# Kernel tuning notes

Measured on AMD Instinct MI355X. Metric: run time of the kernel, lower is better.

## Reference

```python
import jax, jax.numpy as jnp
import numpy as np

N_NODES = 10000
N_EDGES = 640000
D = 128
N_LAYERS = 4


def setup_inputs() -> dict:
    key = jax.random.key(0)
    k1, k2, k3, k4, k5 = jax.random.split(key, 5)
    node_feats = jax.random.normal(k1, (N_NODES, D), dtype=jnp.float32)
    src = jax.random.randint(k2, (N_EDGES,), 0, N_NODES, dtype=jnp.int32)
    dst = jax.random.randint(k3, (N_EDGES,), 0, N_NODES, dtype=jnp.int32)
    # stacked per-layer Linear params (all layers are 128 -> 128)
    Ws = jax.random.normal(k4, (N_LAYERS, D, D), dtype=jnp.float32) / np.sqrt(D).astype(np.float32)
    bs = jax.random.normal(k5, (N_LAYERS, D), dtype=jnp.float32) * 0.01
    return {"node_feats": node_feats, "src": src, "dst": dst, "Ws": Ws, "bs": bs}


def reference(node_feats, src, dst, Ws, bs):
    # Each GCN_layer: h = Linear(x); h = sum_{u in N(v)} h_u  (copy_u/sum)
    # dgl.add_self_loop => aggregate includes the node's own h, i.e. + h.
    # activation = relu; dropout is identity in eval; no batchnorm / residual.
    def step(h, params):
        W, b = params
        hl = h @ W + b                                   # [N, D] dense GEMM
        msgs = hl[src]                                   # [E, D] gather
        agg = jax.ops.segment_sum(msgs, dst, num_segments=N_NODES) + hl  # scatter-sum + self-loop
        return jax.nn.relu(agg), None

    h, _ = jax.lax.scan(step, node_feats, (Ws, bs))
    return h
```

## Files before the change

### kernel.cpp

```cpp
#include <hip/hip_runtime.h>
#include <hip/hip_bf16.h>

#define N_NODES 10000
#define N_EDGES 640000
#define D 128
#define N_LAYERS 4

#define NBINS 79
#define BIN_CAP 10240
#define POISON 0xAAAAAAAAu
#define A_LD 136

typedef unsigned uv4 __attribute__((ext_vector_type(4)));
typedef short bf16x8 __attribute__((ext_vector_type(8)));
typedef float f32x4 __attribute__((ext_vector_type(4)));
typedef float f32x2 __attribute__((ext_vector_type(2)));


__global__ __launch_bounds__(256) void binA_wt_kernel(const int* __restrict__ src,
                                                      const int* __restrict__ dst,
                                                      unsigned* __restrict__ binCursor,
                                                      unsigned* __restrict__ binbuf,
                                                      const float* __restrict__ W,
                                                      unsigned short* __restrict__ Wt) {
    __shared__ int cnt[NBINS];
    __shared__ int gbase[NBINS];
    const int t = threadIdx.x;
    const int b = blockIdx.x;

    if (b >= 250) {
        const int g = (b - 250) * 256 + t;
        const int e0 = g * 8;
        const int l = e0 >> 14;
        const int r = e0 & 16383;
        const int n = r >> 7;
        const int k0 = r & 127;
        union { bf16x8 v; __hip_bfloat16 h[8]; } pk;
#pragma unroll
        for (int j = 0; j < 8; ++j)
            pk.h[j] = __float2bfloat16(W[l * 16384 + (k0 + j) * 128 + n]);
        *(bf16x8*)(Wt + e0) = pk.v;
        return;
    }

    if (t < NBINS) cnt[t] = 0;
    __syncthreads();

    const int e0 = b * 2560;
    unsigned key[10];
    int bin[10], pos[10];
#pragma unroll
    for (int j = 0; j < 10; ++j) {
        int e = e0 + j * 256 + t;
        int d = dst[e];
        int s = src[e];
        key[j] = ((unsigned)d << 14) | (unsigned)s;
        bin[j] = d >> 7;
        pos[j] = atomicAdd(&cnt[bin[j]], 1);
    }
    __syncthreads();
    if (t < NBINS) {
        unsigned old = atomicAdd(&binCursor[t], (unsigned)cnt[t]);
        gbase[t] = (int)(old - POISON);
    }
    __syncthreads();
#pragma unroll
    for (int j = 0; j < 10; ++j) {
        int p = gbase[bin[j]] + pos[j];
        if (p >= 0 && p < BIN_CAP) binbuf[bin[j] * BIN_CAP + p] = key[j];
    }
}


__global__ __launch_bounds__(256) void binB_gemm0_kernel(
        const unsigned* __restrict__ binbuf, const unsigned* __restrict__ binCursor,
        int* __restrict__ begs, int* __restrict__ degs,
        unsigned short* __restrict__ csr16,
        const float* __restrict__ hf, const unsigned short* __restrict__ WtL,
        const float* __restrict__ bias, unsigned short* __restrict__ hl) {
    __shared__ unsigned buf[BIN_CAP];
    __shared__ int deg[128], base[128], cur[128];
    const int b = blockIdx.x;
    const int t = threadIdx.x;

    if (b >= NBINS) {
        const int wave = t >> 6;
        const int lane = t & 63;
        const int ln = lane & 15;
        const int q = lane >> 4;
        const int row0 = (b - NBINS) * 64 + wave * 16;

        int m = row0 + ln;
        if (m > N_NODES - 1) m = N_NODES - 1;

        f32x4 acc[8];
#pragma unroll
        for (int n0 = 0; n0 < 8; ++n0) acc[n0] = (f32x4){0.f, 0.f, 0.f, 0.f};

#pragma unroll
        for (int k0 = 0; k0 < 128; k0 += 32) {
            float4 f0 = *(const float4*)(hf + (size_t)m * D + k0 + q * 8);
            float4 f1 = *(const float4*)(hf + (size_t)m * D + k0 + q * 8 + 4);
            union { bf16x8 v; __hip_bfloat16 b8[8]; } pk;
            pk.b8[0] = __float2bfloat16(f0.x); pk.b8[1] = __float2bfloat16(f0.y);
            pk.b8[2] = __float2bfloat16(f0.z); pk.b8[3] = __float2bfloat16(f0.w);
            pk.b8[4] = __float2bfloat16(f1.x); pk.b8[5] = __float2bfloat16(f1.y);
            pk.b8[6] = __float2bfloat16(f1.z); pk.b8[7] = __float2bfloat16(f1.w);
            bf16x8 a = pk.v;
#pragma unroll
            for (int n0 = 0; n0 < 8; ++n0) {
                bf16x8 bb = *(const bf16x8*)(WtL + (size_t)(n0 * 16 + ln) * D + k0 + q * 8);
                acc[n0] = __builtin_amdgcn_mfma_f32_16x16x32_bf16(a, bb, acc[n0], 0, 0, 0);
            }
        }

#pragma unroll
        for (int n0 = 0; n0 < 8; ++n0) {
            float bv = bias[n0 * 16 + ln];
#pragma unroll
            for (int r = 0; r < 4; ++r) {
                int row = row0 + q * 4 + r;
                if (row < N_NODES) {
                    __hip_bfloat16 o = __float2bfloat16(acc[n0][r] + bv);
                    hl[(size_t)row * D + n0 * 16 + ln] = *(unsigned short*)&o;
                }
            }
        }
        return;
    }

    int m = (int)(binCursor[b] - POISON);
    if (m > BIN_CAP) m = BIN_CAP;
    if (m < 0) m = 0;

    if (t < 128) deg[t] = 0;
    __syncthreads();

    for (int i = t; i < m; i += 256) {
        unsigned k = binbuf[(size_t)b * BIN_CAP + i];
        buf[i] = k;
        atomicAdd(&deg[(k >> 14) & 127], 1);
    }
    __syncthreads();

    if (t < 64) {
        int a0 = deg[2 * t], a1 = deg[2 * t + 1];
        int s = a0 + a1;
        int x = s;
#pragma unroll
        for (int off = 1; off < 64; off <<= 1) {
            int tt = __shfl_up(x, off);
            if (t >= off) x += tt;
        }
        base[2 * t]     = x - s;
        base[2 * t + 1] = x - a1;
        cur[2 * t]      = x - s;
        cur[2 * t + 1]  = x - a1;
    }
    __syncthreads();

    if (t < 128) {
        int v = b * 128 + t;
        if (v < N_NODES) {
            degs[v] = deg[t];
            begs[v] = b * BIN_CAP + base[t];
        }
    }

    for (int i = t; i < m; i += 256) {
        unsigned k = buf[i];
        int p = atomicAdd(&cur[(k >> 14) & 127], 1);
        csr16[(size_t)b * BIN_CAP + p] = (unsigned short)(k & 0x3FFFu);
    }
}

__device__ __forceinline__ float bf_lo(unsigned u) {
    u <<= 16; return __builtin_bit_cast(float, u);
}
__device__ __forceinline__ float bf_hi(unsigned u) {
    u &= 0xffff0000u; return __builtin_bit_cast(float, u);
}
__device__ __forceinline__ f32x2 bf_pair(unsigned u) {
    return (f32x2){bf_lo(u), bf_hi(u)};
}

__device__ __forceinline__ void agg_rows(int node, const uv4* __restrict__ hlq,
                                         const int* __restrict__ begs,
                                         const int* __restrict__ degs,
                                         const unsigned short* __restrict__ csr,
                                         f32x2& a0, f32x2& a1, f32x2& a2, f32x2& a3) {
    const int lane = threadIdx.x & 63;
    const int g = lane >> 4;
    const int c = lane & 15;

    const int beg = begs[node];
    const int end = beg + degs[node];

    a0 = (f32x2){0.f, 0.f}; a1 = a0; a2 = a0; a3 = a0;
    if (g == 0) {
        uv4 sv = hlq[node * 16 + c];
        a0 = bf_pair(sv.x); a1 = bf_pair(sv.y);
        a2 = bf_pair(sv.z); a3 = bf_pair(sv.w);
    }

    int ce0 = beg + lane;
    int cvn = (int)__builtin_nontemporal_load(&csr[ce0 < end ? ce0 : (end - 1)]);
    for (int eb = beg; eb < end; eb += 64) {
        int cv = cvn;
        if (eb + 64 < end) {
            int cen = eb + 64 + lane;
            cvn = (int)__builtin_nontemporal_load(&csr[cen < end ? cen : (end - 1)]);
        }
#pragma unroll
        for (int half = 0; half < 2; ++half) {
            int b0 = eb + 32 * half;
            if (b0 < end) {
#pragma unroll
                for (int j = 0; j < 8; ++j) {
                    int e0 = b0 + 4 * j;
                    if (e0 < end) {
                        int e = e0 + g;
                        int u = __shfl(cv, 32 * half + 4 * j + g);
                        uv4 v = hlq[u * 16 + c];
                        if (e >= end) { v.x = 0u; v.y = 0u; v.z = 0u; v.w = 0u; }
                        a0 += bf_pair(v.x);
                        a1 += bf_pair(v.y);
                        a2 += bf_pair(v.z);
                        a3 += bf_pair(v.w);
                    }
                }
            }
        }
    }

#pragma unroll
    for (int off = 16; off <= 32; off <<= 1) {
        a0.x += __shfl_xor(a0.x, off); a0.y += __shfl_xor(a0.y, off);
        a1.x += __shfl_xor(a1.x, off); a1.y += __shfl_xor(a1.y, off);
        a2.x += __shfl_xor(a2.x, off); a2.y += __shfl_xor(a2.y, off);
        a3.x += __shfl_xor(a3.x, off); a3.y += __shfl_xor(a3.y, off);
    }
}

__global__ __launch_bounds__(1024, 8) void agg_gemm_kernel(
        const uv4* __restrict__ hlq, const int* __restrict__ begs,
        const int* __restrict__ degs, const unsigned short* __restrict__ csr,
        const unsigned short* __restrict__ WtL, const float* __restrict__ bias,
        unsigned short* __restrict__ hlo) {
    __shared__ __hip_bfloat16 Arow[16 * A_LD];
    const int t = threadIdx.x;
    const int wave = t >> 6;
    const int lane = t & 63;
    const int g = lane >> 4;
    const int c = lane & 15;
    const int node = blockIdx.x * 16 + wave;

    f32x2 a0, a1, a2, a3;
    agg_rows(node, hlq, begs, degs, csr, a0, a1, a2, a3);

    if (g == 0) {
        union { bf16x8 v; __hip_bfloat16 h[8]; } pk;
        pk.h[0] = __float2bfloat16(fmaxf(a0.x, 0.f));
        pk.h[1] = __float2bfloat16(fmaxf(a0.y, 0.f));
        pk.h[2] = __float2bfloat16(fmaxf(a1.x, 0.f));
        pk.h[3] = __float2bfloat16(fmaxf(a1.y, 0.f));
        pk.h[4] = __float2bfloat16(fmaxf(a2.x, 0.f));
        pk.h[5] = __float2bfloat16(fmaxf(a2.y, 0.f));
        pk.h[6] = __float2bfloat16(fmaxf(a3.x, 0.f));
        pk.h[7] = __float2bfloat16(fmaxf(a3.y, 0.f));
        *(bf16x8*)&Arow[wave * A_LD + c * 8] = pk.v;
    }
    __syncthreads();

    if (wave < 8) {
        const int ln = lane & 15;
        const int q = lane >> 4;
        f32x4 acc = (f32x4){0.f, 0.f, 0.f, 0.f};
#pragma unroll
        for (int k0 = 0; k0 < 128; k0 += 32) {
            bf16x8 a = *(const bf16x8*)&Arow[ln * A_LD + k0 + q * 8];
            bf16x8 bb = *(const bf16x8*)(WtL + (size_t)(wave * 16 + ln) * D + k0 + q * 8);
            acc = __builtin_amdgcn_mfma_f32_16x16x32_bf16(a, bb, acc, 0, 0, 0);
        }
        float bv = bias[wave * 16 + ln];
#pragma unroll
        for (int r = 0; r < 4; ++r) {
            int row = blockIdx.x * 16 + q * 4 + r;
            __hip_bfloat16 o = __float2bfloat16(acc[r] + bv);
            __builtin_nontemporal_store(*(unsigned short*)&o,
                                        &hlo[(size_t)row * D + wave * 16 + ln]);
        }
    }
}

__global__ __launch_bounds__(256) void agg_final_kernel(const uv4* __restrict__ hlq,
                                                        const int* __restrict__ begs,
                                                        const int* __restrict__ degs,
                                                        const unsigned short* __restrict__ csr,
                                                        float* __restrict__ outf) {
    int node = blockIdx.x * 4 + (threadIdx.x >> 6);
    if (node >= N_NODES) return;
    const int lane = threadIdx.x & 63;
    const int g = lane >> 4;
    const int c = lane & 15;

    f32x2 a0, a1, a2, a3;
    agg_rows(node, hlq, begs, degs, csr, a0, a1, a2, a3);

    if (g == 0) {
        f32x4 o0, o1;
        o0[0] = fmaxf(a0.x, 0.f); o0[1] = fmaxf(a0.y, 0.f);
        o0[2] = fmaxf(a1.x, 0.f); o0[3] = fmaxf(a1.y, 0.f);
        o1[0] = fmaxf(a2.x, 0.f); o1[1] = fmaxf(a2.y, 0.f);
        o1[2] = fmaxf(a3.x, 0.f); o1[3] = fmaxf(a3.y, 0.f);
        f32x4* orow = (f32x4*)(outf + (size_t)node * D);
        __builtin_nontemporal_store(o0, &orow[c * 2]);
        __builtin_nontemporal_store(o1, &orow[c * 2 + 1]);
    }
}


extern "C" void kernel_launch(void* const* d_in, const int* in_sizes, int n_in,
                              void* d_out, int out_size, void* d_ws, size_t ws_size,
                              hipStream_t stream) {
    const float* node_feats = (const float*)d_in[0];
    const int*   src        = (const int*)d_in[1];
    const int*   dst        = (const int*)d_in[2];
    const float* Ws         = (const float*)d_in[3];
    const float* bs         = (const float*)d_in[4];
    float* out = (float*)d_out;

    char* ws = (char*)d_ws;
    unsigned* binCursor     = (unsigned*)(ws + 0);
    int*      begs          = (int*)(ws + 1024);
    int*      degs          = (int*)(ws + 41984);
    unsigned* binbuf        = (unsigned*)(ws + 82944);
    unsigned short* hlA     = (unsigned short*)(ws + 3318784);
    unsigned short* hlB     = (unsigned short*)(ws + 5878784);
    unsigned short* Wt      = (unsigned short*)(ws + 8438784);
    unsigned short* csr16   = (unsigned short*)(ws + 8569856);

    binA_wt_kernel<<<282, 256, 0, stream>>>(src, dst, binCursor, binbuf, Ws, Wt);
    binB_gemm0_kernel<<<NBINS + 157, 256, 0, stream>>>(binbuf, binCursor, begs, degs,
                                                       csr16, node_feats, Wt, bs, hlA);
    agg_gemm_kernel<<<625, 1024, 0, stream>>>((const uv4*)hlA, begs, degs, csr16,
                                              Wt + 1 * 16384, bs + 1 * D, hlB);
    agg_gemm_kernel<<<625, 1024, 0, stream>>>((const uv4*)hlB, begs, degs, csr16,
                                              Wt + 2 * 16384, bs + 2 * D, hlA);
    agg_gemm_kernel<<<625, 1024, 0, stream>>>((const uv4*)hlA, begs, degs, csr16,
                                              Wt + 3 * 16384, bs + 3 * D, hlB);
    agg_final_kernel<<<2500, 256, 0, stream>>>((const uv4*)hlB, begs, degs, csr16, out);
}
```

Measured before the change: 162.5 us.

## Store hidden features as 12-bit per-row-scaled quantized values for gather

Replaces the bf16 intermediate node features with 12-bit offset-quantized values, each row carrying one float scale. The GEMM epilogues compute row abs-max, quantize and pack 8 values into 12 bytes. The aggregation gathers these packed rows, unpacks them and corrects for the zero-point offset. The aim is to cut gather bandwidth from 256 to 192 bytes per row, at the cost of extra shared-memory staging, unpack arithmetic, a per-edge scale load, and possible accuracy loss.

```diff
diff --git a/kernel.cpp b/kernel.cpp
--- a/kernel.cpp
+++ b/kernel.cpp
@@ -10,11 +10,48 @@
 #define BIN_CAP 10240
 #define POISON 0xAAAAAAAAu
 #define A_LD 136
-
-typedef unsigned uv4 __attribute__((ext_vector_type(4)));
+#define ROWB 192
+
 typedef short bf16x8 __attribute__((ext_vector_type(8)));
 typedef float f32x4 __attribute__((ext_vector_type(4)));
 typedef float f32x2 __attribute__((ext_vector_type(2)));
+
+struct U3 { unsigned x, y, z; };
+
+
+__device__ __forceinline__ void unpack_acc(U3 qw, float s,
+                                           f32x2& a0, f32x2& a1, f32x2& a2, f32x2& a3,
+                                           float& bias) {
+    unsigned long long A = (unsigned long long)qw.x | ((unsigned long long)qw.y << 32);
+    unsigned long long B = (unsigned long long)qw.y | ((unsigned long long)qw.z << 32);
+    float q0 = (float)(unsigned)( A        & 0xFFF);
+    float q1 = (float)(unsigned)((A >> 12) & 0xFFF);
+    float q2 = (float)(unsigned)((A >> 24) & 0xFFF);
+    float q3 = (float)(unsigned)((A >> 36) & 0xFFF);
+    float q4 = (float)(unsigned)((A >> 48) & 0xFFF);
+    float q5 = (float)(unsigned)((B >> 28) & 0xFFF);
+    float q6 = (float)(unsigned)((B >> 40) & 0xFFF);
+    float q7 = (float)(unsigned)((B >> 52) & 0xFFF);
+    a0 += (f32x2){q0, q1} * s;
+    a1 += (f32x2){q2, q3} * s;
+    a2 += (f32x2){q4, q5} * s;
+    a3 += (f32x2){q6, q7} * s;
+    bias += s;
+}
+
+__device__ __forceinline__ unsigned quant12(float v, float sinv) {
+    int qi = (int)(v * sinv + 2048.5f);
+    qi = qi < 0 ? 0 : (qi > 4095 ? 4095 : qi);
+    return (unsigned)qi;
+}
+
+__device__ __forceinline__ U3 pack8(const unsigned q[8]) {
+    U3 w;
+    w.x = q[0] | (q[1] << 12) | (q[2] << 24);
+    w.y = (q[2] >> 8) | (q[3] << 4) | (q[4] << 16) | (q[5] << 28);
+    w.z = (q[5] >> 4) | (q[6] << 8) | (q[7] << 20);
+    return w;
+}
 
 
 __global__ __launch_bounds__(256) void binA_wt_kernel(const int* __restrict__ src,
@@ -72,23 +109,31 @@
 }
 
 
+struct K2SMem {
+    union {
+        struct { unsigned buf[BIN_CAP]; int deg[128], base[128], cur[128]; } bb;
+        struct { float Dt[64 * 128]; float smax[64]; } g0;
+    } u;
+};
+
 __global__ __launch_bounds__(256) void binB_gemm0_kernel(
         const unsigned* __restrict__ binbuf, const unsigned* __restrict__ binCursor,
         int* __restrict__ begs, int* __restrict__ degs,
         unsigned short* __restrict__ csr16,
         const float* __restrict__ hf, const unsigned short* __restrict__ WtL,
-        const float* __restrict__ bias, unsigned short* __restrict__ hl) {
-    __shared__ unsigned buf[BIN_CAP];
-    __shared__ int deg[128], base[128], cur[128];
+        const float* __restrict__ bias, unsigned char* __restrict__ hl12,
+        float* __restrict__ scaleOut) {
+    __shared__ K2SMem sm;
     const int b = blockIdx.x;
     const int t = threadIdx.x;
 
     if (b >= NBINS) {
+        const int tile = b - NBINS;
         const int wave = t >> 6;
         const int lane = t & 63;
         const int ln = lane & 15;
         const int q = lane >> 4;
-        const int row0 = (b - NBINS) * 64 + wave * 16;
+        const int row0 = tile * 64 + wave * 16;
 
         int m = row0 + ln;
         if (m > N_NODES - 1) m = N_NODES - 1;
@@ -118,13 +163,44 @@
         for (int n0 = 0; n0 < 8; ++n0) {
             float bv = bias[n0 * 16 + ln];
 #pragma unroll
-            for (int r = 0; r < 4; ++r) {
-                int row = row0 + q * 4 + r;
-                if (row < N_NODES) {
-                    __hip_bfloat16 o = __float2bfloat16(acc[n0][r] + bv);
-                    hl[(size_t)row * D + n0 * 16 + ln] = *(unsigned short*)&o;
-                }
-            }
+            for (int r = 0; r < 4; ++r) acc[n0][r] += bv;
+        }
+#pragma unroll
+        for (int r = 0; r < 4; ++r) {
+            float mx = 0.f;
+#pragma unroll
+            for (int n0 = 0; n0 < 8; ++n0) mx = fmaxf(mx, fabsf(acc[n0][r]));
+            mx = fmaxf(mx, __shfl_xor(mx, 1));
+            mx = fmaxf(mx, __shfl_xor(mx, 2));
+            mx = fmaxf(mx, __shfl_xor(mx, 4));
+            mx = fmaxf(mx, __shfl_xor(mx, 8));
+            if (ln == 0) sm.u.g0.smax[wave * 16 + q * 4 + r] = mx;
+        }
+#pragma unroll
+        for (int n0 = 0; n0 < 8; ++n0)
+#pragma unroll
+            for (int r = 0; r < 4; ++r)
+                sm.u.g0.Dt[(wave * 16 + q * 4 + r) * 128 + n0 * 16 + ln] = acc[n0][r];
+        __syncthreads();
+
+        const int ln16 = t & 15;
+        const int rbase = t >> 4;
+#pragma unroll
+        for (int rr = 0; rr < 4; ++rr) {
+            int row = rbase + rr * 16;
+            int grow = tile * 64 + row;
+            float mx = sm.u.g0.smax[row];
+            float sinv = mx > 0.f ? 2047.f / mx : 0.f;
+            unsigned qv[8];
+#pragma unroll
+            for (int j = 0; j < 8; ++j)
+                qv[j] = quant12(sm.u.g0.Dt[row * 128 + ln16 * 8 + j], sinv);
+            if (grow < N_NODES)
+                *(U3*)(hl12 + (size_t)grow * ROWB + ln16 * 12) = pack8(qv);
+        }
+        if (t < 64) {
+            int grow = tile * 64 + t;
+            if (grow < N_NODES) scaleOut[grow] = sm.u.g0.smax[t] * (1.f / 2047.f);
         }
         return;
     }
@@ -133,18 +209,18 @@
     if (m > BIN_CAP) m = BIN_CAP;
     if (m < 0) m = 0;
 
-    if (t < 128) deg[t] = 0;
+    if (t < 128) sm.u.bb.deg[t] = 0;
     __syncthreads();
 
     for (int i = t; i < m; i += 256) {
         unsigned k = binbuf[(size_t)b * BIN_CAP + i];
-        buf[i] = k;
-        atomicAdd(&deg[(k >> 14) & 127], 1);
+        sm.u.bb.buf[i] = k;
+        atomicAdd(&sm.u.bb.deg[(k >> 14) & 127], 1);
     }
     __syncthreads();
 
     if (t < 64) {
-        int a0 = deg[2 * t], a1 = deg[2 * t + 1];
+        int a0 = sm.u.bb.deg[2 * t], a1 = sm.u.bb.deg[2 * t + 1];
         int s = a0 + a1;
         int x = s;
 #pragma unroll
@@ -152,43 +228,35 @@
             int tt = __shfl_up(x, off);
             if (t >= off) x += tt;
         }
-        base[2 * t]     = x - s;
-        base[2 * t + 1] = x - a1;
-        cur[2 * t]      = x - s;
-        cur[2 * t + 1]  = x - a1;
+        sm.u.bb.base[2 * t]     = x - s;
+        sm.u.bb.base[2 * t + 1] = x - a1;
+        sm.u.bb.cur[2 * t]      = x - s;
+        sm.u.bb.cur[2 * t + 1]  = x - a1;
     }
     __syncthreads();
 
     if (t < 128) {
         int v = b * 128 + t;
         if (v < N_NODES) {
-            degs[v] = deg[t];
-            begs[v] = b * BIN_CAP + base[t];
+            degs[v] = sm.u.bb.deg[t];
+            begs[v] = b * BIN_CAP + sm.u.bb.base[t];
         }
     }
 
     for (int i = t; i < m; i += 256) {
-        unsigned k = buf[i];
-        int p = atomicAdd(&cur[(k >> 14) & 127], 1);
+        unsigned k = sm.u.bb.buf[i];
+        int p = atomicAdd(&sm.u.bb.cur[(k >> 14) & 127], 1);
         csr16[(size_t)b * BIN_CAP + p] = (unsigned short)(k & 0x3FFFu);
     }
 }
 
-__device__ __forceinline__ float bf_lo(unsigned u) {
-    u <<= 16; return __builtin_bit_cast(float, u);
-}
-__device__ __forceinline__ float bf_hi(unsigned u) {
-    u &= 0xffff0000u; return __builtin_bit_cast(float, u);
-}
-__device__ __forceinline__ f32x2 bf_pair(unsigned u) {
-    return (f32x2){bf_lo(u), bf_hi(u)};
-}
-
-__device__ __forceinline__ void agg_rows(int node, const uv4* __restrict__ hlq,
-                                         const int* __restrict__ begs,
-                                         const int* __restrict__ degs,
-                                         const unsigned short* __restrict__ csr,
-                                         f32x2& a0, f32x2& a1, f32x2& a2, f32x2& a3) {
+__device__ __forceinline__ void agg_rows12(int node,
+                                           const unsigned char* __restrict__ hl12,
+                                           const float* __restrict__ sc,
+                                           const int* __restrict__ begs,
+                                           const int* __restrict__ degs,
+                                           const unsigned short* __restrict__ csr,
+                                           f32x2& a0, f32x2& a1, f32x2& a2, f32x2& a3) {
     const int lane = threadIdx.x & 63;
     const int g = lane >> 4;
     const int c = lane & 15;
@@ -197,10 +265,10 @@
     const int end = beg + degs[node];
 
     a0 = (f32x2){0.f, 0.f}; a1 = a0; a2 = a0; a3 = a0;
+    float bias = 0.f;
     if (g == 0) {
-        uv4 sv = hlq[node * 16 + c];
-        a0 = bf_pair(sv.x); a1 = bf_pair(sv.y);
-        a2 = bf_pair(sv.z); a3 = bf_pair(sv.w);
+        U3 qw = *(const U3*)(hl12 + (size_t)node * ROWB + c * 12);
+        unpack_acc(qw, sc[node], a0, a1, a2, a3, bias);
     }
 
     int ce0 = beg + lane;
@@ -221,12 +289,10 @@
                     if (e0 < end) {
                         int e = e0 + g;
                         int u = __shfl(cv, 32 * half + 4 * j + g);
-                        uv4 v = hlq[u * 16 + c];
-                        if (e >= end) { v.x = 0u; v.y = 0u; v.z = 0u; v.w = 0u; }
-                        a0 += bf_pair(v.x);
-                        a1 += bf_pair(v.y);
-                        a2 += bf_pair(v.z);
-                        a3 += bf_pair(v.w);
+                        U3 qw = *(const U3*)(hl12 + (size_t)u * ROWB + c * 12);
+                        float s = sc[u];
+                        if (e >= end) s = 0.f;
+                        unpack_acc(qw, s, a0, a1, a2, a3, bias);
                     }
                 }
             }
@@ -239,25 +305,35 @@
         a1.x += __shfl_xor(a1.x, off); a1.y += __shfl_xor(a1.y, off);
         a2.x += __shfl_xor(a2.x, off); a2.y += __shfl_xor(a2.y, off);
         a3.x += __shfl_xor(a3.x, off); a3.y += __shfl_xor(a3.y, off);
-    }
+        bias += __shfl_xor(bias, off);
+    }
+    const float corr = 2048.f * bias;
+    a0.x -= corr; a0.y -= corr; a1.x -= corr; a1.y -= corr;
+    a2.x -= corr; a2.y -= corr; a3.x -= corr; a3.y -= corr;
 }
 
 __global__ __launch_bounds__(1024, 8) void agg_gemm_kernel(
-        const uv4* __restrict__ hlq, const int* __restrict__ begs,
-        const int* __restrict__ degs, const unsigned short* __restrict__ csr,
+        const unsigned char* __restrict__ hl12, const float* __restrict__ sc,
+        const int* __restrict__ begs, const int* __restrict__ degs,
+        const unsigned short* __restrict__ csr,
         const unsigned short* __restrict__ WtL, const float* __restrict__ bias,
-        unsigned short* __restrict__ hlo) {
+        unsigned char* __restrict__ hlo12, float* __restrict__ scaleOut) {
     __shared__ __hip_bfloat16 Arow[16 * A_LD];
+    __shared__ float Dt[16 * 128];
+    __shared__ unsigned rowmaxu[16];
+    __shared__ float sinv16[16];
     const int t = threadIdx.x;
     const int wave = t >> 6;
     const int lane = t & 63;
     const int g = lane >> 4;
     const int c = lane & 15;
-    const int node = blockIdx.x * 16 + wave;
+    const int node0 = blockIdx.x * 16;
+    const int node = node0 + wave;
 
     f32x2 a0, a1, a2, a3;
-    agg_rows(node, hlq, begs, degs, csr, a0, a1, a2, a3);
-
+    agg_rows12(node, hl12, sc, begs, degs, csr, a0, a1, a2, a3);
+
+    if (t < 16) rowmaxu[t] = 0u;
     if (g == 0) {
         union { bf16x8 v; __hip_bfloat16 h[8]; } pk;
         pk.h[0] = __float2bfloat16(fmaxf(a0.x, 0.f));
@@ -284,20 +360,43 @@
         }
         float bv = bias[wave * 16 + ln];
 #pragma unroll
+        for (int r = 0; r < 4; ++r) acc[r] += bv;
+#pragma unroll
         for (int r = 0; r < 4; ++r) {
-            int row = blockIdx.x * 16 + q * 4 + r;
-            __hip_bfloat16 o = __float2bfloat16(acc[r] + bv);
-            __builtin_nontemporal_store(*(unsigned short*)&o,
-                                        &hlo[(size_t)row * D + wave * 16 + ln]);
-        }
-    }
-}
-
-__global__ __launch_bounds__(256) void agg_final_kernel(const uv4* __restrict__ hlq,
-                                                        const int* __restrict__ begs,
-                                                        const int* __restrict__ degs,
-                                                        const unsigned short* __restrict__ csr,
-                                                        float* __restrict__ outf) {
+            float mx = fabsf(acc[r]);
+            mx = fmaxf(mx, __shfl_xor(mx, 1));
+            mx = fmaxf(mx, __shfl_xor(mx, 2));
+            mx = fmaxf(mx, __shfl_xor(mx, 4));
+            mx = fmaxf(mx, __shfl_xor(mx, 8));
+            if (ln == 0) atomicMax(&rowmaxu[q * 4 + r], __float_as_uint(mx));
+            Dt[(q * 4 + r) * 128 + wave * 16 + ln] = acc[r];
+        }
+    }
+    __syncthreads();
+
+    if (t < 16) {
+        float mx = __uint_as_float(rowmaxu[t]);
+        sinv16[t] = mx > 0.f ? 2047.f / mx : 0.f;
+        scaleOut[node0 + t] = mx * (1.f / 2047.f);
+    }
+    __syncthreads();
+
+    if (t < 256) {
+        const int ln16 = t & 15;
+        const int row = t >> 4;
+        float sinv = sinv16[row];
+        unsigned qv[8];
+#pragma unroll
+        for (int j = 0; j < 8; ++j)
+            qv[j] = quant12(Dt[row * 128 + ln16 * 8 + j], sinv);
+        *(U3*)(hlo12 + (size_t)(node0 + row) * ROWB + ln16 * 12) = pack8(qv);
+    }
+}
+
+__global__ __launch_bounds__(256) void agg_final_kernel(
+        const unsigned char* __restrict__ hl12, const float* __restrict__ sc,
+        const int* __restrict__ begs, const int* __restrict__ degs,
+        const unsigned short* __restrict__ csr, float* __restrict__ outf) {
     int node = blockIdx.x * 4 + (threadIdx.x >> 6);
     if (node >= N_NODES) return;
     const int lane = threadIdx.x & 63;
@@ -305,7 +404,7 @@
     const int c = lane & 15;
 
     f32x2 a0, a1, a2, a3;
-    agg_rows(node, hlq, begs, degs, csr, a0, a1, a2, a3);
+    agg_rows12(node, hl12, sc, begs, degs, csr, a0, a1, a2, a3);
 
     if (g == 0) {
         f32x4 o0, o1;
@@ -335,19 +434,25 @@
     int*      begs          = (int*)(ws + 1024);
     int*      degs          = (int*)(ws + 41984);
     unsigned* binbuf        = (unsigned*)(ws + 82944);
-    unsigned short* hlA     = (unsigned short*)(ws + 3318784);
-    unsigned short* hlB     = (unsigned short*)(ws + 5878784);
-    unsigned short* Wt      = (unsigned short*)(ws + 8438784);
-    unsigned short* csr16   = (unsigned short*)(ws + 8569856);
+    unsigned short* csr16   = (unsigned short*)(ws + 3318784);
+    unsigned char*  hl12A   = (unsigned char*)(ws + 4936704);
+    unsigned char*  hl12B   = (unsigned char*)(ws + 6856704);
+    float*    scaleA        = (float*)(ws + 8776704);
+    float*    scaleB        = (float*)(ws + 8816704);
+    unsigned short* Wt      = (unsigned short*)(ws + 8856704);
 
     binA_wt_kernel<<<282, 256, 0, stream>>>(src, dst, binCursor, binbuf, Ws, Wt);
     binB_gemm0_kernel<<<NBINS + 157, 256, 0, stream>>>(binbuf, binCursor, begs, degs,
-                                                       csr16, node_feats, Wt, bs, hlA);
-    agg_gemm_kernel<<<625, 1024, 0, stream>>>((const uv4*)hlA, begs, degs, csr16,
-                                              Wt + 1 * 16384, bs + 1 * D, hlB);
-    agg_gemm_kernel<<<625, 1024, 0, stream>>>((const uv4*)hlB, begs, degs, csr16,
-                                              Wt + 2 * 16384, bs + 2 * D, hlA);
-    agg_gemm_kernel<<<625, 1024, 0, stream>>>((const uv4*)hlA, begs, degs, csr16,
-                                              Wt + 3 * 16384, bs + 3 * D, hlB);
-    agg_final_kernel<<<2500, 256, 0, stream>>>((const uv4*)hlB, begs, degs, csr16, out);
-}
+                                                       csr16, node_feats, Wt, bs,
+                                                       hl12A, scaleA);
+    agg_gemm_kernel<<<625, 1024, 0, stream>>>(hl12A, scaleA, begs, degs, csr16,
+                                              Wt + 1 * 16384, bs + 1 * D,
+                                              hl12B, scaleB);
+    agg_gemm_kernel<<<625, 1024, 0, stream>>>(hl12B, scaleB, begs, degs, csr16,
+                                              Wt + 2 * 16384, bs + 2 * D,
+                                              hl12A, scaleA);
+    agg_gemm_kernel<<<625, 1024, 0, stream>>>(hl12A, scaleA, begs, degs, csr16,
+                                              Wt + 3 * 16384, bs + 3 * D,
+                                              hl12B, scaleB);
+    agg_final_kernel<<<2500, 256, 0, stream>>>(hl12B, scaleB, begs, degs, csr16, out);
+}
```

Measured after the change: 177.4 us. 9.1% more time.

## Split each node's neighbor aggregation across two waves and combine partials in LDS

Applied to the files above, without the earlier changes.

Each node's edge range is now split in half, with two waves gathering neighbor rows and the second wave's partial sum merged through shared memory before ReLU. The fused aggregate+GEMM kernel now handles 8 nodes per block instead of 16, padding the unused MFMA rows with zeros, and launches twice as many blocks. The aim is more gather parallelism and more memory-level concurrency per node, at the cost of extra syncs and LDS traffic and half-empty MFMA tiles. The workspace layout is also reordered.

```diff
diff --git a/kernel.cpp b/kernel.cpp
--- a/kernel.cpp
+++ b/kernel.cpp
@@ -184,49 +184,47 @@
     return (f32x2){bf_lo(u), bf_hi(u)};
 }
 
-__device__ __forceinline__ void agg_rows(int node, const uv4* __restrict__ hlq,
-                                         const int* __restrict__ begs,
-                                         const int* __restrict__ degs,
-                                         const unsigned short* __restrict__ csr,
-                                         f32x2& a0, f32x2& a1, f32x2& a2, f32x2& a3) {
+__device__ __forceinline__ void agg_range(const uv4* __restrict__ hlq,
+                                          int selfnode, int beg, int end,
+                                          const unsigned short* __restrict__ csr,
+                                          f32x2& a0, f32x2& a1, f32x2& a2, f32x2& a3) {
     const int lane = threadIdx.x & 63;
     const int g = lane >> 4;
     const int c = lane & 15;
 
-    const int beg = begs[node];
-    const int end = beg + degs[node];
-
     a0 = (f32x2){0.f, 0.f}; a1 = a0; a2 = a0; a3 = a0;
-    if (g == 0) {
-        uv4 sv = hlq[node * 16 + c];
+    if (selfnode >= 0 && g == 0) {
+        uv4 sv = hlq[selfnode * 16 + c];
         a0 = bf_pair(sv.x); a1 = bf_pair(sv.y);
         a2 = bf_pair(sv.z); a3 = bf_pair(sv.w);
     }
 
-    int ce0 = beg + lane;
-    int cvn = (int)__builtin_nontemporal_load(&csr[ce0 < end ? ce0 : (end - 1)]);
-    for (int eb = beg; eb < end; eb += 64) {
-        int cv = cvn;
-        if (eb + 64 < end) {
-            int cen = eb + 64 + lane;
-            cvn = (int)__builtin_nontemporal_load(&csr[cen < end ? cen : (end - 1)]);
-        }
-#pragma unroll
-        for (int half = 0; half < 2; ++half) {
-            int b0 = eb + 32 * half;
-            if (b0 < end) {
-#pragma unroll
-                for (int j = 0; j < 8; ++j) {
-                    int e0 = b0 + 4 * j;
-                    if (e0 < end) {
-                        int e = e0 + g;
-                        int u = __shfl(cv, 32 * half + 4 * j + g);
-                        uv4 v = hlq[u * 16 + c];
-                        if (e >= end) { v.x = 0u; v.y = 0u; v.z = 0u; v.w = 0u; }
-                        a0 += bf_pair(v.x);
-                        a1 += bf_pair(v.y);
-                        a2 += bf_pair(v.z);
-                        a3 += bf_pair(v.w);
+    if (beg < end) {
+        int ce0 = beg + lane;
+        int cvn = (int)__builtin_nontemporal_load(&csr[ce0 < end ? ce0 : (end - 1)]);
+        for (int eb = beg; eb < end; eb += 64) {
+            int cv = cvn;
+            if (eb + 64 < end) {
+                int cen = eb + 64 + lane;
+                cvn = (int)__builtin_nontemporal_load(&csr[cen < end ? cen : (end - 1)]);
+            }
+#pragma unroll
+            for (int half = 0; half < 2; ++half) {
+                int b0 = eb + 32 * half;
+                if (b0 < end) {
+#pragma unroll
+                    for (int j = 0; j < 8; ++j) {
+                        int e0 = b0 + 4 * j;
+                        if (e0 < end) {
+                            int e = e0 + g;
+                            int u = __shfl(cv, 32 * half + 4 * j + g);
+                            uv4 v = hlq[u * 16 + c];
+                            if (e >= end) { v.x = 0u; v.y = 0u; v.z = 0u; v.w = 0u; }
+                            a0 += bf_pair(v.x);
+                            a1 += bf_pair(v.y);
+                            a2 += bf_pair(v.z);
+                            a3 += bf_pair(v.w);
+                        }
                     }
                 }
             }
@@ -242,33 +240,54 @@
     }
 }
 
-__global__ __launch_bounds__(1024, 8) void agg_gemm_kernel(
+__global__ __launch_bounds__(1024, 8) void agg2_gemm_kernel(
         const uv4* __restrict__ hlq, const int* __restrict__ begs,
         const int* __restrict__ degs, const unsigned short* __restrict__ csr,
         const unsigned short* __restrict__ WtL, const float* __restrict__ bias,
         unsigned short* __restrict__ hlo) {
     __shared__ __hip_bfloat16 Arow[16 * A_LD];
+    __shared__ float Part[8][128];
     const int t = threadIdx.x;
     const int wave = t >> 6;
     const int lane = t & 63;
     const int g = lane >> 4;
     const int c = lane & 15;
-    const int node = blockIdx.x * 16 + wave;
+    const int nl = wave >> 1;
+    const int h = wave & 1;
+    const int node0 = blockIdx.x * 8;
+    const int node = node0 + nl;
+
+    for (int i = t; i < 8 * A_LD; i += 1024)
+        Arow[8 * A_LD + i] = __float2bfloat16(0.f);
+
+    const int beg = degs ? begs[node] : 0;
+    const int dg = degs[node];
+    const int hf = (dg + 1) >> 1;
+    const int rb = h ? beg + hf : beg;
+    const int re = h ? beg + dg : beg + hf;
 
     f32x2 a0, a1, a2, a3;
-    agg_rows(node, hlq, begs, degs, csr, a0, a1, a2, a3);
-
-    if (g == 0) {
-        union { bf16x8 v; __hip_bfloat16 h[8]; } pk;
-        pk.h[0] = __float2bfloat16(fmaxf(a0.x, 0.f));
-        pk.h[1] = __float2bfloat16(fmaxf(a0.y, 0.f));
-        pk.h[2] = __float2bfloat16(fmaxf(a1.x, 0.f));
-        pk.h[3] = __float2bfloat16(fmaxf(a1.y, 0.f));
-        pk.h[4] = __float2bfloat16(fmaxf(a2.x, 0.f));
-        pk.h[5] = __float2bfloat16(fmaxf(a2.y, 0.f));
-        pk.h[6] = __float2bfloat16(fmaxf(a3.x, 0.f));
-        pk.h[7] = __float2bfloat16(fmaxf(a3.y, 0.f));
-        *(bf16x8*)&Arow[wave * A_LD + c * 8] = pk.v;
+    agg_range(hlq, h == 0 ? node : -1, rb, re, csr, a0, a1, a2, a3);
+
+    if (h == 1 && g == 0) {
+        Part[nl][0 * 16 + c] = a0.x; Part[nl][1 * 16 + c] = a0.y;
+        Part[nl][2 * 16 + c] = a1.x; Part[nl][3 * 16 + c] = a1.y;
+        Part[nl][4 * 16 + c] = a2.x; Part[nl][5 * 16 + c] = a2.y;
+        Part[nl][6 * 16 + c] = a3.x; Part[nl][7 * 16 + c] = a3.y;
+    }
+    __syncthreads();
+
+    if (h == 0 && g == 0) {
+        union { bf16x8 v; __hip_bfloat16 hh[8]; } pk;
+        pk.hh[0] = __float2bfloat16(fmaxf(a0.x + Part[nl][0 * 16 + c], 0.f));
+        pk.hh[1] = __float2bfloat16(fmaxf(a0.y + Part[nl][1 * 16 + c], 0.f));
+        pk.hh[2] = __float2bfloat16(fmaxf(a1.x + Part[nl][2 * 16 + c], 0.f));
+        pk.hh[3] = __float2bfloat16(fmaxf(a1.y + Part[nl][3 * 16 + c], 0.f));
+        pk.hh[4] = __float2bfloat16(fmaxf(a2.x + Part[nl][4 * 16 + c], 0.f));
+        pk.hh[5] = __float2bfloat16(fmaxf(a2.y + Part[nl][5 * 16 + c], 0.f));
+        pk.hh[6] = __float2bfloat16(fmaxf(a3.x + Part[nl][6 * 16 + c], 0.f));
+        pk.hh[7] = __float2bfloat16(fmaxf(a3.y + Part[nl][7 * 16 + c], 0.f));
+        *(bf16x8*)&Arow[nl * A_LD + c * 8] = pk.v;
     }
     __syncthreads();
 
@@ -285,34 +304,57 @@
         float bv = bias[wave * 16 + ln];
 #pragma unroll
         for (int r = 0; r < 4; ++r) {
-            int row = blockIdx.x * 16 + q * 4 + r;
-            __hip_bfloat16 o = __float2bfloat16(acc[r] + bv);
-            __builtin_nontemporal_store(*(unsigned short*)&o,
-                                        &hlo[(size_t)row * D + wave * 16 + ln]);
-        }
-    }
-}
-
-__global__ __launch_bounds__(256) void agg_final_kernel(const uv4* __restrict__ hlq,
-                                                        const int* __restrict__ begs,
-                                                        const int* __restrict__ degs,
-                                                        const unsigned short* __restrict__ csr,
-                                                        float* __restrict__ outf) {
-    int node = blockIdx.x * 4 + (threadIdx.x >> 6);
-    if (node >= N_NODES) return;
-    const int lane = threadIdx.x & 63;
+            int row = q * 4 + r;
+            if (row < 8) {
+                __hip_bfloat16 o = __float2bfloat16(acc[r] + bv);
+                __builtin_nontemporal_store(*(unsigned short*)&o,
+                                            &hlo[(size_t)(node0 + row) * D + wave * 16 + ln]);
+            }
+        }
+    }
+}
+
+__global__ __launch_bounds__(256) void agg_final2_kernel(
+        const uv4* __restrict__ hlq, const int* __restrict__ begs,
+        const int* __restrict__ degs, const unsigned short* __restrict__ csr,
+        float* __restrict__ outf) {
+    __shared__ float Part[2][128];
+    const int t = threadIdx.x;
+    const int wave = t >> 6;
+    const int lane = t & 63;
     const int g = lane >> 4;
     const int c = lane & 15;
+    const int nl = wave >> 1;
+    const int h = wave & 1;
+    const int node = blockIdx.x * 2 + nl;
+
+    const int beg = begs[node];
+    const int dg = degs[node];
+    const int hf = (dg + 1) >> 1;
+    const int rb = h ? beg + hf : beg;
+    const int re = h ? beg + dg : beg + hf;
 
     f32x2 a0, a1, a2, a3;
-    agg_rows(node, hlq, begs, degs, csr, a0, a1, a2, a3);
-
-    if (g == 0) {
+    agg_range(hlq, h == 0 ? node : -1, rb, re, csr, a0, a1, a2, a3);
+
+    if (h == 1 && g == 0) {
+        Part[nl][0 * 16 + c] = a0.x; Part[nl][1 * 16 + c] = a0.y;
+        Part[nl][2 * 16 + c] = a1.x; Part[nl][3 * 16 + c] = a1.y;
+        Part[nl][4 * 16 + c] = a2.x; Part[nl][5 * 16 + c] = a2.y;
+        Part[nl][6 * 16 + c] = a3.x; Part[nl][7 * 16 + c] = a3.y;
+    }
+    __syncthreads();
+
+    if (h == 0 && g == 0) {
         f32x4 o0, o1;
-        o0[0] = fmaxf(a0.x, 0.f); o0[1] = fmaxf(a0.y, 0.f);
-        o0[2] = fmaxf(a1.x, 0.f); o0[3] = fmaxf(a1.y, 0.f);
-        o1[0] = fmaxf(a2.x, 0.f); o1[1] = fmaxf(a2.y, 0.f);
-        o1[2] = fmaxf(a3.x, 0.f); o1[3] = fmaxf(a3.y, 0.f);
+        o0[0] = fmaxf(a0.x + Part[nl][0 * 16 + c], 0.f);
+        o0[1] = fmaxf(a0.y + Part[nl][1 * 16 + c], 0.f);
+        o0[2] = fmaxf(a1.x + Part[nl][2 * 16 + c], 0.f);
+        o0[3] = fmaxf(a1.y + Part[nl][3 * 16 + c], 0.f);
+        o1[0] = fmaxf(a2.x + Part[nl][4 * 16 + c], 0.f);
+        o1[1] = fmaxf(a2.y + Part[nl][5 * 16 + c], 0.f);
+        o1[2] = fmaxf(a3.x + Part[nl][6 * 16 + c], 0.f);
+        o1[3] = fmaxf(a3.y + Part[nl][7 * 16 + c], 0.f);
         f32x4* orow = (f32x4*)(outf + (size_t)node * D);
         __builtin_nontemporal_store(o0, &orow[c * 2]);
         __builtin_nontemporal_store(o1, &orow[c * 2 + 1]);
@@ -335,19 +377,19 @@
     int*      begs          = (int*)(ws + 1024);
     int*      degs          = (int*)(ws + 41984);
     unsigned* binbuf        = (unsigned*)(ws + 82944);
-    unsigned short* hlA     = (unsigned short*)(ws + 3318784);
-    unsigned short* hlB     = (unsigned short*)(ws + 5878784);
-    unsigned short* Wt      = (unsigned short*)(ws + 8438784);
-    unsigned short* csr16   = (unsigned short*)(ws + 8569856);
+    unsigned short* csr16   = (unsigned short*)(ws + 3318784);
+    unsigned short* hlA     = (unsigned short*)(ws + 4936704);
+    unsigned short* hlB     = (unsigned short*)(ws + 7496704);
+    unsigned short* Wt      = (unsigned short*)(ws + 10056704);
 
     binA_wt_kernel<<<282, 256, 0, stream>>>(src, dst, binCursor, binbuf, Ws, Wt);
     binB_gemm0_kernel<<<NBINS + 157, 256, 0, stream>>>(binbuf, binCursor, begs, degs,
                                                        csr16, node_feats, Wt, bs, hlA);
-    agg_gemm_kernel<<<625, 1024, 0, stream>>>((const uv4*)hlA, begs, degs, csr16,
-                                              Wt + 1 * 16384, bs + 1 * D, hlB);
-    agg_gemm_kernel<<<625, 1024, 0, stream>>>((const uv4*)hlB, begs, degs, csr16,
-                                              Wt + 2 * 16384, bs + 2 * D, hlA);
-    agg_gemm_kernel<<<625, 1024, 0, stream>>>((const uv4*)hlA, begs, degs, csr16,
-                                              Wt + 3 * 16384, bs + 3 * D, hlB);
-    agg_final_kernel<<<2500, 256, 0, stream>>>((const uv4*)hlB, begs, degs, csr16, out);
-}
+    agg2_gemm_kernel<<<1250, 1024, 0, stream>>>((const uv4*)hlA, begs, degs, csr16,
+                                                Wt + 1 * 16384, bs + 1 * D, hlB);
+    agg2_gemm_kernel<<<1250, 1024, 0, stream>>>((const uv4*)hlB, begs, degs, csr16,
+                                                Wt + 2 * 16384, bs + 2 * D, hlA);
+    agg2_gemm_kernel<<<1250, 1024, 0, stream>>>((const uv4*)hlA, begs, degs, csr16,
+                                                Wt + 3 * 16384, bs + 3 * D, hlB);
+    agg_final2_kernel<<<5000, 256, 0, stream>>>((const uv4*)hlB, begs, degs, csr16, out);
+}
```

Result: slower. 173.2 us (+6.6%).
